# Kernel tuning notes

Measured on AMD Instinct MI355X. Metric: run time of the kernel, lower is better.

Reference implementation:

```python
import jax, jax.numpy as jnp
import numpy as np
import math

D = 2048
NH = 16       # query heads
NKV = 4       # kv heads (GQA)
HD = 128
SOFTCLAMP = 50.0
ROPE_BASE = 10000.0
B = 4
SQ_VLM = 1024
SQ_ACT = 64
S_CACHE = 256


def _heads(x, n):
    # [B,S,n*HD] -> [B,n,S,HD]
    b, s, _ = x.shape
    return x.reshape(b, s, n, HD).transpose(0, 2, 1, 3)


def _rope_cos_sin(pos):
    # pos: [B,S] int -> cos,sin [B,1,S,HD]
    inv_freq = 1.0 / (ROPE_BASE ** (jnp.arange(0, HD, 2, dtype=jnp.float32) / HD))
    freqs = pos.astype(jnp.float32)[..., None] * inv_freq  # [B,S,HD/2]
    emb = jnp.concatenate([freqs, freqs], axis=-1)         # [B,S,HD]
    return jnp.cos(emb)[:, None], jnp.sin(emb)[:, None]


def _apply_rope(x, cos, sin):
    # x: [B,H,S,HD]
    x1, x2 = x[..., : HD // 2], x[..., HD // 2 :]
    rot = jnp.concatenate([-x2, x1], axis=-1)
    return x * cos + rot * sin


def setup_inputs() -> dict:
    key = jax.random.key(0)
    ks = jax.random.split(key, 16)
    sc = lambda d: 1.0 / math.sqrt(d)
    inp = {
        'attention_mask': jnp.zeros((B, 1, SQ_VLM + SQ_ACT, S_CACHE + SQ_VLM + SQ_ACT), jnp.float32),
        'pos_vlm': jnp.broadcast_to(jnp.arange(S_CACHE, S_CACHE + SQ_VLM, dtype=jnp.int32), (B, SQ_VLM)),
        'pos_action': jnp.broadcast_to(jnp.arange(S_CACHE + SQ_VLM, S_CACHE + SQ_VLM + SQ_ACT, dtype=jnp.int32), (B, SQ_ACT)),
        'h_vlm': jax.random.normal(ks[0], (B, SQ_VLM, D), jnp.float32),
        'h_action': jax.random.normal(ks[1], (B, SQ_ACT, D), jnp.float32),
        'k_cache': jax.random.normal(ks[2], (B, NKV, S_CACHE, HD), jnp.float32),
        'v_cache': jax.random.normal(ks[3], (B, NKV, S_CACHE, HD), jnp.float32),
        'Wq_vlm': jax.random.normal(ks[4], (D, NH * HD), jnp.float32) * sc(D),
        'Wk_vlm': jax.random.normal(ks[5], (D, NKV * HD), jnp.float32) * sc(D),
        'Wv_vlm': jax.random.normal(ks[6], (D, NKV * HD), jnp.float32) * sc(D),
        'Wq_act': jax.random.normal(ks[7], (D, NH * HD), jnp.float32) * sc(D),
        'Wk_act': jax.random.normal(ks[8], (D, NKV * HD), jnp.float32) * sc(D),
        'Wv_act': jax.random.normal(ks[9], (D, NKV * HD), jnp.float32) * sc(D),
        'Wo_act': jax.random.normal(ks[10], (NH * HD, D), jnp.float32) * sc(NH * HD),
    }
    return inp


def reference(attention_mask, pos_vlm, pos_action, h_vlm, h_action, k_cache, v_cache,
              Wq_vlm, Wk_vlm, Wv_vlm, Wq_act, Wk_act, Wv_act, Wo_act):
    group = NH // NKV

    def qkv(h, pos, Wq, Wk, Wv):
        q = _heads(h @ Wq, NH)
        k = _heads(h @ Wk, NKV)
        v = _heads(h @ Wv, NKV)
        cos, sin = _rope_cos_sin(pos)
        return _apply_rope(q, cos, sin), _apply_rope(k, cos, sin), v

    q_v, k_v, v_v = qkv(h_vlm, pos_vlm, Wq_vlm, Wk_vlm, Wv_vlm)
    q_a, k_a, v_a = qkv(h_action, pos_action, Wq_act, Wk_act, Wv_act)

    # repeat_kv (GQA) on every KV source, cached mixture first (append_non_active order)
    rep = lambda t: jnp.repeat(t, group, axis=1)  # [B,NKV,S,HD] -> [B,NH,S,HD]
    k = jnp.concatenate([rep(k_cache), rep(k_v), rep(k_a)], axis=2)
    v = jnp.concatenate([rep(v_cache), rep(v_v), rep(v_a)], axis=2)
    q = jnp.concatenate([q_v, q_a], axis=2)  # [B,NH,Sq,HD]

    scores = jnp.einsum('bhqd,bhkd->bhqk', q, k) / math.sqrt(HD)
    scores = jnp.tanh(scores / SOFTCLAMP) * SOFTCLAMP + attention_mask
    w = jax.nn.softmax(scores.astype(jnp.float32), axis=-1).astype(q.dtype)
    out = jnp.einsum('bhqk,bhkd->bhqd', w, v)
    out = out.transpose(0, 2, 1, 3).reshape(B, SQ_VLM + SQ_ACT, NH * HD)

    # split by q_lens; 'vlm' is in post_attn_skip_names -> no o_proj, dropped
    out_action = out[:, SQ_VLM:, :]
    return out_action @ Wo_act
```

## Files before the change

kernel.cpp:

```cpp
#include <hip/hip_runtime.h>
#include <cmath>

#define NH 16
#define NKV 4
#define HD 128
#define DMODEL 2048
#define BB 4
#define SQV 1024
#define SQA 64
#define SCACHE 256
#define STOT 1344
#define SQTOT 1088
#define NSPLIT 21

typedef unsigned short u16;
typedef __attribute__((ext_vector_type(8))) short short8;
typedef __attribute__((ext_vector_type(4))) float f32x4;

__device__ __forceinline__ float b2f(u16 u) {
    union { float f; unsigned int i; } x; x.i = ((unsigned int)u) << 16; return x.f;
}
__device__ __forceinline__ u16 f2b(float f) {
    unsigned int x = __float_as_uint(f);
    x = x + 0x7fffu + ((x >> 16) & 1u);
    return (u16)(x >> 16);
}

__device__ __forceinline__ void gload16(const void* g, void* l) {
    __builtin_amdgcn_global_load_lds((const __attribute__((address_space(1))) void*)g,
                                     (__attribute__((address_space(3))) void*)l, 16, 0, 0);
}

__device__ __forceinline__ void transpose_body(const float* in, u16* out, int N,
                                               int bx, int by) {
    __shared__ __align__(16) u16 t[64 * 66];
    int n0 = bx * 64, k0 = by * 64;
    int tid = threadIdx.x;
    int r = tid >> 3;
    int c8 = (tid & 7) * 8;
#pragma unroll
    for (int h = 0; h < 2; h++) {
        int k = r + h * 32;
        const float* f = in + (size_t)(k0 + k) * N + n0 + c8;
        float4 a = *(const float4*)f, b = *(const float4*)(f + 4);
        u16 vv[8] = {f2b(a.x), f2b(a.y), f2b(a.z), f2b(a.w),
                     f2b(b.x), f2b(b.y), f2b(b.z), f2b(b.w)};
#pragma unroll
        for (int j = 0; j < 8; j++) t[(c8 + j) * 66 + k] = vv[j];
    }
    __syncthreads();
#pragma unroll
    for (int h = 0; h < 2; h++) {
        int n = r + h * 32;
        short8 v;
#pragma unroll
        for (int j = 0; j < 8; j++) ((u16*)&v)[j] = t[n * 66 + c8 + j];
        *(short8*)(out + (size_t)(n0 + n) * 2048 + k0 + c8) = v;
    }
}

__device__ __forceinline__ void transpose_vc(const float* vc, u16* VT, int idx) {
    __shared__ __align__(16) u16 tv[64 * 66];
    int bkv = idx >> 3, t8 = idx & 7;
    int key0 = (t8 >> 1) * 64, d0 = (t8 & 1) * 64;
    const float* in = vc + ((size_t)bkv * SCACHE + key0) * HD + d0;
    u16* out = VT + ((size_t)bkv * HD + d0) * STOT + key0;
    int tid = threadIdx.x;
    int r = tid >> 3, c8 = (tid & 7) * 8;
#pragma unroll
    for (int h = 0; h < 2; h++) {
        int k = r + h * 32;
        const float* f = in + (size_t)k * HD + c8;
        float4 a = *(const float4*)f, b = *(const float4*)(f + 4);
        u16 vv[8] = {f2b(a.x), f2b(a.y), f2b(a.z), f2b(a.w),
                     f2b(b.x), f2b(b.y), f2b(b.z), f2b(b.w)};
#pragma unroll
        for (int j = 0; j < 8; j++) tv[(c8 + j) * 66 + k] = vv[j];
    }
    __syncthreads();
#pragma unroll
    for (int h = 0; h < 2; h++) {
        int d = r + h * 32;
        short8 v;
#pragma unroll
        for (int j = 0; j < 8; j++) ((u16*)&v)[j] = tv[d * 66 + c8 + j];
        *(short8*)(out + (size_t)d * STOT + c8) = v;
    }
}

__global__ void k_prep(const float* __restrict__ mask,
                       const float* __restrict__ kc, const float* __restrict__ vc,
                       const float* __restrict__ hv, const float* __restrict__ ha,
                       const float* __restrict__ w0, u16* __restrict__ o0,
                       const float* __restrict__ w1, u16* __restrict__ o1,
                       const float* __restrict__ w2, u16* __restrict__ o2,
                       const float* __restrict__ w3, u16* __restrict__ o3,
                       const float* __restrict__ w4, u16* __restrict__ o4,
                       const float* __restrict__ w5, u16* __restrict__ o5,
                       float* __restrict__ cosT, float* __restrict__ sinT,
                       u16* __restrict__ maskS, u16* __restrict__ K_all, u16* __restrict__ VT_all,
                       u16* __restrict__ hv16, u16* __restrict__ ha16) {
    int gx = blockIdx.x, tid = threadIdx.x;
    if (gx < 3072) {
        if (gx < 256)        transpose_body(w0, o0, 512,  gx & 7,  gx >> 3);
        else if (gx < 512)   { int g = gx - 256;  transpose_body(w1, o1, 512,  g & 7,  g >> 3); }
        else if (gx < 768)   { int g = gx - 512;  transpose_body(w2, o2, 512,  g & 7,  g >> 3); }
        else if (gx < 1024)  { int g = gx - 768;  transpose_body(w3, o3, 512,  g & 7,  g >> 3); }
        else if (gx < 2048)  { int g = gx - 1024; transpose_body(w4, o4, 2048, g & 31, g >> 5); }
        else                 { int g = gx - 2048; transpose_body(w5, o5, 2048, g & 31, g >> 5); }
        return;
    }
    int bx = gx - 3072;
    if (bx < 336) {
        int i = bx * 256 + tid;
        if (i < STOT * 64) {
            int p = i >> 6, j = i & 63;
            float inv = __expf(-(float)j * (9.210340371976184f / 64.0f));
            float ang = (float)p * inv;
            cosT[i] = cosf(ang);
            sinT[i] = sinf(ang);
        }
    } else if (bx < 1680) {
        int i = (bx - 336) * 256 + tid;
        int b = i / (SQA * STOT);
        int r = i % (SQA * STOT);
        size_t s = (size_t)b * SQTOT * STOT + (size_t)SQV * STOT + r;
        maskS[i] = f2b(mask[s]);
    } else if (bx < 1936) {
        int i = (bx - 1680) * 256 + tid;
        int e = i * 8;
        int bk = e / (SCACHE * HD);
        int off = e % (SCACHE * HD);
        size_t dst = (size_t)bk * STOT * HD + off;
        const float* fk = kc + e;
        u16 tk[8];
#pragma unroll
        for (int j = 0; j < 8; j++) tk[j] = f2b(fk[j]);
        *(short8*)(K_all + dst) = *(short8*)tk;
    } else if (bx < 6032) {
        int i = (bx - 1936) * 256 + tid;
        int e = i * 8;
        const float* f = hv + e;
        float4 a = *(const float4*)f, b = *(const float4*)(f + 4);
        u16 t[8] = {f2b(a.x), f2b(a.y), f2b(a.z), f2b(a.w),
                    f2b(b.x), f2b(b.y), f2b(b.z), f2b(b.w)};
        *(short8*)(hv16 + e) = *(short8*)t;
    } else if (bx < 6288) {
        int i = (bx - 6032) * 256 + tid;
        int e = i * 8;
        const float* f = ha + e;
        float4 a = *(const float4*)f, b = *(const float4*)(f + 4);
        u16 t[8] = {f2b(a.x), f2b(a.y), f2b(a.z), f2b(a.w),
                    f2b(b.x), f2b(b.y), f2b(b.z), f2b(b.w)};
        *(short8*)(ha16 + e) = *(short8*)t;
    } else {
        transpose_vc(vc, VT_all, bx - 6288);
    }
}

__global__ __launch_bounds__(256) void k_gemm_qkv(
    const u16* __restrict__ Avlm, const u16* __restrict__ Aact,
    const u16* __restrict__ WkvT, const u16* __restrict__ WvvT,
    const u16* __restrict__ WqaT, const u16* __restrict__ WkaT, const u16* __restrict__ WvaT,
    const int* __restrict__ pos_vlm, const int* __restrict__ pos_act,
    const float* __restrict__ cosT, const float* __restrict__ sinT,
    u16* __restrict__ Qbuf, u16* __restrict__ K_all, u16* __restrict__ VT_all) {
    __shared__ __align__(16) u16 smem[2 * 12288];
    int tid = threadIdx.x;
    int w = tid >> 6, lane = tid & 63;
    int la = lane & 15, lg = lane >> 4;
    int wm = (w & 1) * 32;
    int c2 = w >> 1;
    int ntab[4] = {c2 * 2, c2 * 2 + 1, c2 * 2 + 4, c2 * 2 + 5};

    const u16* A; const u16* Bt; int m0, n0;
    int path;
    int head;
    int bid = blockIdx.x;
    if (bid < 512) {
        m0 = (bid & 63) * 64;
        int yy = bid >> 6;
        path = (yy < 4) ? 0 : 1;
        head = yy & 3;
        n0 = head * 128;
        A = Avlm;
        Bt = (path == 0) ? WkvT : WvvT;
    } else {
        int g = bid - 512;
        m0 = (g & 3) * 64;
        int ny = g >> 2;
        A = Aact;
        if (ny < 16)      { path = 2; head = ny;      Bt = WqaT; n0 = ny * 128; }
        else if (ny < 20) { path = 3; head = ny - 16; Bt = WkaT; n0 = (ny - 16) * 128; }
        else              { path = 4; head = ny - 20; Bt = WvaT; n0 = (ny - 20) * 128; }
    }

    f32x4 acc[2][4];
#pragma unroll
    for (int i = 0; i < 2; i++)
#pragma unroll
        for (int j = 0; j < 4; j++) acc[i][j] = (f32x4){0.f, 0.f, 0.f, 0.f};

    int srow = tid >> 3;
    int scsrc = (((tid & 7) * 16) ^ ((srow & 7) << 4)) >> 1;

#define STAGE_QKV(CB, KB) do {                                                        \
        u16* Ab_ = smem + (CB) * 12288;                                               \
        u16* Bb_ = Ab_ + 4096;                                                        \
        _Pragma("unroll")                                                             \
        for (int h = 0; h < 2; h++)                                                   \
            gload16(A + (size_t)(m0 + srow + h * 32) * DMODEL + (KB) + scsrc,         \
                    Ab_ + h * 2048 + tid * 8);                                        \
        _Pragma("unroll")                                                             \
        for (int h = 0; h < 4; h++)                                                   \
            gload16(Bt + (size_t)(n0 + srow + h * 32) * DMODEL + (KB) + scsrc,        \
                    Bb_ + h * 2048 + tid * 8);                                        \
    } while (0)

    STAGE_QKV(0, 0);
    int cur = 0;
    int swr = (la & 7) << 3;
    for (int kb = 0; kb < DMODEL; kb += 64) {
        if (kb + 64 < DMODEL) {
            STAGE_QKV(cur ^ 1, kb + 64);
            asm volatile("s_waitcnt vmcnt(6)" ::: "memory");
        } else {
            asm volatile("s_waitcnt vmcnt(0)" ::: "memory");
        }
        __builtin_amdgcn_s_barrier();
        asm volatile("" ::: "memory");
        const u16* Ac = smem + cur * 12288;
        const u16* Bc = Ac + 4096;
#pragma unroll
        for (int kk = 0; kk < 2; kk++) {
            short8 af[2], bf[4];
            int cc = (kk * 32 + lg * 8) ^ swr;
#pragma unroll
            for (int mt = 0; mt < 2; mt++)
                af[mt] = *(const short8*)&Ac[(wm + mt * 16 + la) * 64 + cc];
#pragma unroll
            for (int nt = 0; nt < 4; nt++)
                bf[nt] = *(const short8*)&Bc[(ntab[nt] * 16 + la) * 64 + cc];
#pragma unroll
            for (int mt = 0; mt < 2; mt++)
#pragma unroll
                for (int nt = 0; nt < 4; nt++)
                    acc[mt][nt] = __builtin_amdgcn_mfma_f32_16x16x32_bf16(af[mt], bf[nt], acc[mt][nt], 0, 0, 0);
        }
        __builtin_amdgcn_s_barrier();
        cur ^= 1;
    }
#undef STAGE_QKV

#pragma unroll
    for (int mt = 0; mt < 2; mt++) {
#pragma unroll
        for (int r = 0; r < 4; r++) {
            int gm = m0 + wm + mt * 16 + lg * 4 + r;
            if (path <= 1) {
                int b = gm >> 10, s = gm & 1023;
                if (path == 0) {
                    size_t base = ((size_t)(b * NKV + head) * STOT + SCACHE + s) * HD;
                    int pos = pos_vlm[gm];
#pragma unroll
                    for (int i = 0; i < 2; i++) {
                        int dlo = ntab[i] * 16 + la;
                        float x1 = acc[mt][i][r], x2 = acc[mt][i + 2][r];
                        float cs = cosT[pos * 64 + dlo], sn = sinT[pos * 64 + dlo];
                        K_all[base + dlo]      = f2b(x1 * cs - x2 * sn);
                        K_all[base + dlo + 64] = f2b(x2 * cs + x1 * sn);
                    }
                } else {
                    size_t vt = ((size_t)(b * NKV + head) * HD) * STOT + SCACHE + s;
#pragma unroll
                    for (int i = 0; i < 4; i++) {
                        int d = ntab[i] * 16 + la;
                        VT_all[vt + (size_t)d * STOT] = f2b(acc[mt][i][r]);
                    }
                }
            } else {
                int b = gm >> 6, s = gm & 63;
                if (path == 2) {
                    int pos = pos_act[gm];
                    size_t qb = ((size_t)(b * NH + head) * SQA + s) * HD;
#pragma unroll
                    for (int i = 0; i < 2; i++) {
                        int dlo = ntab[i] * 16 + la;
                        float x1 = acc[mt][i][r], x2 = acc[mt][i + 2][r];
                        float cs = cosT[pos * 64 + dlo], sn = sinT[pos * 64 + dlo];
                        Qbuf[qb + dlo]      = f2b(x1 * cs - x2 * sn);
                        Qbuf[qb + dlo + 64] = f2b(x2 * cs + x1 * sn);
                    }
                } else if (path == 3) {
                    int pos = pos_act[gm];
                    size_t base = ((size_t)(b * NKV + head) * STOT + SCACHE + SQV + s) * HD;
#pragma unroll
                    for (int i = 0; i < 2; i++) {
                        int dlo = ntab[i] * 16 + la;
                        float x1 = acc[mt][i][r], x2 = acc[mt][i + 2][r];
                        float cs = cosT[pos * 64 + dlo], sn = sinT[pos * 64 + dlo];
                        K_all[base + dlo]      = f2b(x1 * cs - x2 * sn);
                        K_all[base + dlo + 64] = f2b(x2 * cs + x1 * sn);
                    }
                } else {
                    size_t vt = ((size_t)(b * NKV + head) * HD) * STOT + SCACHE + SQV + s;
#pragma unroll
                    for (int i = 0; i < 4; i++) {
                        int d = ntab[i] * 16 + la;
                        VT_all[vt + (size_t)d * STOT] = f2b(acc[mt][i][r]);
                    }
                }
            }
        }
    }
}

__global__ __launch_bounds__(256) void k_attn_split(
    const u16* __restrict__ Qbuf, const u16* __restrict__ K_all, const u16* __restrict__ VT_all,
    const u16* __restrict__ maskS, u16* __restrict__ po, float* __restrict__ pml) {
    int h = blockIdx.x, b = blockIdx.y, p = blockIdx.z;
    int bh = b * NH + h;
    int kvh = h >> 2;
    const u16* Kb  = K_all  + (size_t)(b * NKV + kvh) * STOT * HD;
    const u16* VTb = VT_all + (size_t)(b * NKV + kvh) * HD * STOT;
    const u16* Qb  = Qbuf + (size_t)bh * SQA * HD;
    int tid = threadIdx.x, w = tid >> 6, lane = tid & 63;
    int la = lane & 15, lg = lane >> 4;
    __shared__ __align__(16) u16 Ks[64 * 128];
    __shared__ __align__(16) u16 Vt[128 * 64];
    __shared__ __align__(16) u16 Ps[4][16 * 72];

    int kr = tid >> 4;
    int ksw = (((tid & 15) * 16) ^ ((kr & 7) << 4)) >> 1;
    int vr = tid >> 3;
    int vsw = (((tid & 7) * 16) ^ ((vr & 7) << 4)) >> 1;
#pragma unroll
    for (int hh = 0; hh < 4; hh++)
        gload16(Kb + (size_t)(p * 64 + kr + hh * 16) * HD + ksw, &Ks[hh * 2048 + tid * 8]);
#pragma unroll
    for (int hh = 0; hh < 4; hh++)
        gload16(VTb + (size_t)(vr + hh * 32) * STOT + p * 64 + vsw, &Vt[hh * 2048 + tid * 8]);

    short8 qf[4];
#pragma unroll
    for (int kk = 0; kk < 4; kk++)
        qf[kk] = *(const short8*)(Qb + (size_t)(w * 16 + la) * HD + kk * 32 + lg * 8);
    u16 mreg[4][4];
#pragma unroll
    for (int nt = 0; nt < 4; nt++)
#pragma unroll
        for (int r = 0; r < 4; r++)
            mreg[nt][r] = maskS[((size_t)(b * SQA + w * 16 + lg * 4 + r)) * STOT +
                                p * 64 + nt * 16 + la];

    asm volatile("s_waitcnt vmcnt(0)" ::: "memory");
    __builtin_amdgcn_s_barrier();
    asm volatile("" ::: "memory");

    int swr = (la & 7) << 3;
    const float scl = 0.08838834764831845f;
    f32x4 s_acc[4];
#pragma unroll
    for (int nt = 0; nt < 4; nt++) s_acc[nt] = (f32x4){0.f, 0.f, 0.f, 0.f};
    __builtin_amdgcn_s_setprio(1);
#pragma unroll
    for (int kk = 0; kk < 4; kk++) {
        int cc = (kk * 32 + lg * 8) ^ swr;
#pragma unroll
        for (int nt = 0; nt < 4; nt++) {
            short8 kf = *(const short8*)&Ks[(nt * 16 + la) * 128 + cc];
            s_acc[nt] = __builtin_amdgcn_mfma_f32_16x16x32_bf16(qf[kk], kf, s_acc[nt], 0, 0, 0);
        }
    }
    __builtin_amdgcn_s_setprio(0);
    float sc[4][4];
#pragma unroll
    for (int nt = 0; nt < 4; nt++) {
#pragma unroll
        for (int r = 0; r < 4; r++) {
            float sv = s_acc[nt][r] * scl;
            float x = sv * 0.02f;
            float t = __expf(-2.0f * fabsf(x));
            float th = __fdividef(1.0f - t, 1.0f + t);
            sv = copysignf(th, x) * 50.0f;
            sv += b2f(mreg[nt][r]);
            sc[nt][r] = sv;
        }
    }
    float m_fin[4], l_fin[4];
#pragma unroll
    for (int r = 0; r < 4; r++) {
        float mx = fmaxf(fmaxf(sc[0][r], sc[1][r]), fmaxf(sc[2][r], sc[3][r]));
#pragma unroll
        for (int sh = 1; sh < 16; sh <<= 1) mx = fmaxf(mx, __shfl_xor(mx, sh, 64));
        float rowsum = 0.f;
#pragma unroll
        for (int nt = 0; nt < 4; nt++) {
            float pv = __expf(sc[nt][r] - mx);
            Ps[w][(lg * 4 + r) * 72 + nt * 16 + la] = f2b(pv);
            rowsum += pv;
        }
#pragma unroll
        for (int sh = 1; sh < 16; sh <<= 1) rowsum += __shfl_xor(rowsum, sh, 64);
        m_fin[r] = mx;
        l_fin[r] = rowsum;
    }
    f32x4 o_acc[8];
#pragma unroll
    for (int nt = 0; nt < 8; nt++) o_acc[nt] = (f32x4){0.f, 0.f, 0.f, 0.f};
    __builtin_amdgcn_s_setprio(1);
#pragma unroll
    for (int kk = 0; kk < 2; kk++) {
        short8 pf = *(const short8*)&Ps[w][la * 72 + kk * 32 + lg * 8];
        int cc = (kk * 32 + lg * 8) ^ swr;
#pragma unroll
        for (int nt = 0; nt < 8; nt++) {
            short8 vf = *(const short8*)&Vt[(nt * 16 + la) * 64 + cc];
            o_acc[nt] = __builtin_amdgcn_mfma_f32_16x16x32_bf16(pf, vf, o_acc[nt], 0, 0, 0);
        }
    }
    __builtin_amdgcn_s_setprio(0);
#pragma unroll
    for (int nt = 0; nt < 8; nt++) {
#pragma unroll
        for (int r = 0; r < 4; r++) {
            int sq = w * 16 + lg * 4 + r;
            po[(((size_t)p * 64 + bh) * 64 + sq) * 128 + nt * 16 + la] = f2b(o_acc[nt][r]);
        }
    }
    if (la == 0) {
#pragma unroll
        for (int r = 0; r < 4; r++) {
            int sq = w * 16 + lg * 4 + r;
            size_t mlb = (((size_t)p * 64 + bh) * 64 + sq) * 2;
            pml[mlb] = m_fin[r];
            pml[mlb + 1] = l_fin[r];
        }
    }
}

__global__ __launch_bounds__(256) void k_attn_red(
    const u16* __restrict__ po, const float* __restrict__ pml, u16* __restrict__ AO) {
    int h = blockIdx.x, b = blockIdx.y, qz = blockIdx.z * 16;
    int bh = b * NH + h;
    __shared__ float wgt[NSPLIT][16];
    int tid = threadIdx.x;
    if (tid < 16) {
        int q = qz + tid;
        float m[NSPLIT], l[NSPLIT], M = -3e38f;
#pragma unroll
        for (int p = 0; p < NSPLIT; p++) {
            size_t mlb = (((size_t)p * 64 + bh) * 64 + q) * 2;
            m[p] = pml[mlb]; l[p] = pml[mlb + 1];
            M = fmaxf(M, m[p]);
        }
        float L = 0.f;
#pragma unroll
        for (int p = 0; p < NSPLIT; p++) L += l[p] * __expf(m[p] - M);
        float inv = 1.0f / L;
#pragma unroll
        for (int p = 0; p < NSPLIT; p++) wgt[p][tid] = __expf(m[p] - M) * inv;
    }
    __syncthreads();
    for (int e = tid; e < 16 * 128; e += 256) {
        int q = qz + (e >> 7), d = e & 127;
        float s = 0.f;
#pragma unroll
        for (int p = 0; p < NSPLIT; p++)
            s += b2f(po[(((size_t)p * 64 + bh) * 64 + q) * 128 + d]) * wgt[p][e >> 7];
        AO[((size_t)(b * SQA + q)) * 2048 + h * HD + d] = f2b(s);
    }
}

__global__ __launch_bounds__(256) void k_gemm_out(
    const u16* __restrict__ A, const u16* __restrict__ WoT, float* __restrict__ out) {
    __shared__ __align__(16) u16 smem[2 * 6144];
    int m0 = blockIdx.x * 32, n0 = blockIdx.y * 64;
    int tid = threadIdx.x;
    int w = tid >> 6, lane = tid & 63;
    int la = lane & 15, lg = lane >> 4;
    int wm = (w & 1) * 16, wn = (w >> 1) * 32;
    f32x4 acc[2];
#pragma unroll
    for (int j = 0; j < 2; j++) acc[j] = (f32x4){0.f, 0.f, 0.f, 0.f};

    int srow = tid >> 3;
    int scsrc = (((tid & 7) * 16) ^ ((srow & 7) << 4)) >> 1;

#define STAGE_OUT(CB, KB) do {                                                        \
        u16* Ab_ = smem + (CB) * 6144;                                                \
        u16* Bb_ = Ab_ + 2048;                                                        \
        gload16(A + (size_t)(m0 + srow) * DMODEL + (KB) + scsrc, Ab_ + tid * 8);      \
        _Pragma("unroll")                                                             \
        for (int h = 0; h < 2; h++)                                                   \
            gload16(WoT + (size_t)(n0 + srow + h * 32) * DMODEL + (KB) + scsrc,       \
                    Bb_ + h * 2048 + tid * 8);                                        \
    } while (0)

    STAGE_OUT(0, 0);
    int cur = 0;
    int swr = (la & 7) << 3;
    for (int kb = 0; kb < DMODEL; kb += 64) {
        if (kb + 64 < DMODEL) {
            STAGE_OUT(cur ^ 1, kb + 64);
            asm volatile("s_waitcnt vmcnt(3)" ::: "memory");
        } else {
            asm volatile("s_waitcnt vmcnt(0)" ::: "memory");
        }
        __builtin_amdgcn_s_barrier();
        asm volatile("" ::: "memory");
        const u16* Ac = smem + cur * 6144;
        const u16* Bc = Ac + 2048;
#pragma unroll
        for (int kk = 0; kk < 2; kk++) {
            int cc = (kk * 32 + lg * 8) ^ swr;
            short8 af = *(const short8*)&Ac[(wm + la) * 64 + cc];
            short8 bf[2];
#pragma unroll
            for (int nt = 0; nt < 2; nt++) bf[nt] = *(const short8*)&Bc[(wn + nt * 16 + la) * 64 + cc];
#pragma unroll
            for (int nt = 0; nt < 2; nt++)
                acc[nt] = __builtin_amdgcn_mfma_f32_16x16x32_bf16(af, bf[nt], acc[nt], 0, 0, 0);
        }
        __builtin_amdgcn_s_barrier();
        cur ^= 1;
    }
#undef STAGE_OUT

#pragma unroll
    for (int r = 0; r < 4; r++) {
        int gm = m0 + wm + lg * 4 + r;
#pragma unroll
        for (int nt = 0; nt < 2; nt++)
            out[(size_t)gm * DMODEL + n0 + wn + nt * 16 + la] = acc[nt][r];
    }
}

extern "C" void kernel_launch(void* const* d_in, const int* in_sizes, int n_in,
                              void* d_out, int out_size, void* d_ws, size_t ws_size,
                              hipStream_t stream) {
    (void)in_sizes; (void)n_in; (void)out_size;
    const float* mask    = (const float*)d_in[0];
    const int*   pos_vlm = (const int*)d_in[1];
    const int*   pos_act = (const int*)d_in[2];
    const float* h_vlm   = (const float*)d_in[3];
    const float* h_act   = (const float*)d_in[4];
    const float* k_cache = (const float*)d_in[5];
    const float* v_cache = (const float*)d_in[6];
    const float* Wk_vlm  = (const float*)d_in[8];
    const float* Wv_vlm  = (const float*)d_in[9];
    const float* Wq_act  = (const float*)d_in[10];
    const float* Wk_act  = (const float*)d_in[11];
    const float* Wv_act  = (const float*)d_in[12];
    const float* Wo_act  = (const float*)d_in[13];

    const size_t NEED = 80183296;
    if (ws_size < NEED) return;
    char* ws = (char*)d_ws;
    float* cosT  = (float*)(ws + 0);
    float* sinT  = (float*)(ws + 344064);
    u16* K_all   = (u16*)(ws + 688128);
    u16* VT_all  = (u16*)(ws + 6193152);
    u16* Qbuf    = (u16*)(ws + 11698176);
    u16* AO      = (u16*)(ws + 12746752);
    u16* WkvT    = (u16*)(ws + 13795328);
    u16* WvvT    = (u16*)(ws + 15892480);
    u16* WqaT    = (u16*)(ws + 17989632);
    u16* WkaT    = (u16*)(ws + 26378240);
    u16* WvaT    = (u16*)(ws + 28475392);
    u16* WoT     = (u16*)(ws + 30572544);
    u16* po      = (u16*)(ws + 38961152);
    float* pml   = (float*)(ws + 60981248);
    u16* maskS   = (u16*)(ws + 61669376);
    u16* hv16    = (u16*)(ws + 62357504);
    u16* ha16    = (u16*)(ws + 79134720);

    hipLaunchKernelGGL(k_prep, dim3(9488), dim3(256), 0, stream,
                       mask, k_cache, v_cache, h_vlm, h_act,
                       Wk_vlm, WkvT, Wv_vlm, WvvT, Wk_act, WkaT, Wv_act, WvaT,
                       Wq_act, WqaT, Wo_act, WoT,
                       cosT, sinT, maskS, K_all, VT_all, hv16, ha16);
    hipLaunchKernelGGL(k_gemm_qkv, dim3(608), dim3(256), 0, stream,
                       hv16, ha16, WkvT, WvvT, WqaT, WkaT, WvaT,
                       pos_vlm, pos_act, cosT, sinT, Qbuf, K_all, VT_all);
    hipLaunchKernelGGL(k_attn_split, dim3(16, 4, NSPLIT), dim3(256), 0, stream,
                       Qbuf, K_all, VT_all, maskS, po, pml);
    hipLaunchKernelGGL(k_attn_red, dim3(16, 4, 4), dim3(256), 0, stream, po, pml, AO);
    hipLaunchKernelGGL(k_gemm_out, dim3(8, 32), dim3(256), 0, stream, AO, WoT, (float*)d_out);
}
```

Measured before the change: 232.7 us.

## Triple-buffer QKV GEMM and loop attention splits over three KV chunks

The QKV GEMM switches from double to triple buffering, issuing loads two stages ahead and dropping the trailing barrier per iteration. The split attention kernel now processes three 64-key chunks per block with online softmax (lazy rescale when the max grows by more than 8) and double-buffered K/V staging, cutting splits from 21 to 7. This reduces partial-output traffic and the reduction work, but gives fewer attention blocks and more LDS per GEMM block, which may lower occupancy.

```diff
diff --git a/kernel.cpp b/kernel.cpp
--- a/kernel.cpp
+++ b/kernel.cpp
@@ -11,7 +11,7 @@
 #define SCACHE 256
 #define STOT 1344
 #define SQTOT 1088
-#define NSPLIT 21
+#define NSPLIT 7
 
 typedef unsigned short u16;
 typedef __attribute__((ext_vector_type(8))) short short8;
@@ -165,7 +165,7 @@
     const int* __restrict__ pos_vlm, const int* __restrict__ pos_act,
     const float* __restrict__ cosT, const float* __restrict__ sinT,
     u16* __restrict__ Qbuf, u16* __restrict__ K_all, u16* __restrict__ VT_all) {
-    __shared__ __align__(16) u16 smem[2 * 12288];
+    __shared__ __align__(16) u16 smem[3 * 12288];
     int tid = threadIdx.x;
     int w = tid >> 6, lane = tid & 63;
     int la = lane & 15, lg = lane >> 4;
@@ -204,8 +204,8 @@
     int srow = tid >> 3;
     int scsrc = (((tid & 7) * 16) ^ ((srow & 7) << 4)) >> 1;
 
-#define STAGE_QKV(CB, KB) do {                                                        \
-        u16* Ab_ = smem + (CB) * 12288;                                               \
+#define STAGE_QKV(BASE, KB) do {                                                      \
+        u16* Ab_ = (BASE);                                                            \
         u16* Bb_ = Ab_ + 4096;                                                        \
         _Pragma("unroll")                                                             \
         for (int h = 0; h < 2; h++)                                                   \
@@ -217,19 +217,17 @@
                     Bb_ + h * 2048 + tid * 8);                                        \
     } while (0)
 
-    STAGE_QKV(0, 0);
-    int cur = 0;
+    STAGE_QKV(smem, 0);
+    STAGE_QKV(smem + 12288, 64);
+    int bufR = 0, bufS = 2;
     int swr = (la & 7) << 3;
-    for (int kb = 0; kb < DMODEL; kb += 64) {
-        if (kb + 64 < DMODEL) {
-            STAGE_QKV(cur ^ 1, kb + 64);
-            asm volatile("s_waitcnt vmcnt(6)" ::: "memory");
-        } else {
-            asm volatile("s_waitcnt vmcnt(0)" ::: "memory");
-        }
+    for (int t = 0; t < 32; ++t) {
+        if (t < 31) asm volatile("s_waitcnt vmcnt(6)" ::: "memory");
+        else        asm volatile("s_waitcnt vmcnt(0)" ::: "memory");
         __builtin_amdgcn_s_barrier();
         asm volatile("" ::: "memory");
-        const u16* Ac = smem + cur * 12288;
+        if (t < 30) STAGE_QKV(smem + bufS * 12288, (t + 2) * 64);
+        const u16* Ac = smem + bufR * 12288;
         const u16* Bc = Ac + 4096;
 #pragma unroll
         for (int kk = 0; kk < 2; kk++) {
@@ -247,8 +245,8 @@
                 for (int nt = 0; nt < 4; nt++)
                     acc[mt][nt] = __builtin_amdgcn_mfma_f32_16x16x32_bf16(af[mt], bf[nt], acc[mt][nt], 0, 0, 0);
         }
-        __builtin_amdgcn_s_barrier();
-        cur ^= 1;
+        bufR = (bufR == 2) ? 0 : bufR + 1;
+        bufS = (bufS == 2) ? 0 : bufS + 1;
     }
 #undef STAGE_QKV
 
@@ -326,100 +324,125 @@
     const u16* Qb  = Qbuf + (size_t)bh * SQA * HD;
     int tid = threadIdx.x, w = tid >> 6, lane = tid & 63;
     int la = lane & 15, lg = lane >> 4;
-    __shared__ __align__(16) u16 Ks[64 * 128];
-    __shared__ __align__(16) u16 Vt[128 * 64];
+    __shared__ __align__(16) u16 Ks[2][64 * 128];
+    __shared__ __align__(16) u16 Vt[2][128 * 64];
     __shared__ __align__(16) u16 Ps[4][16 * 72];
 
     int kr = tid >> 4;
     int ksw = (((tid & 15) * 16) ^ ((kr & 7) << 4)) >> 1;
     int vr = tid >> 3;
     int vsw = (((tid & 7) * 16) ^ ((vr & 7) << 4)) >> 1;
-#pragma unroll
-    for (int hh = 0; hh < 4; hh++)
-        gload16(Kb + (size_t)(p * 64 + kr + hh * 16) * HD + ksw, &Ks[hh * 2048 + tid * 8]);
-#pragma unroll
-    for (int hh = 0; hh < 4; hh++)
-        gload16(VTb + (size_t)(vr + hh * 32) * STOT + p * 64 + vsw, &Vt[hh * 2048 + tid * 8]);
-
+
+#define ASTAGE(CB, G) do {                                                            \
+        _Pragma("unroll")                                                             \
+        for (int hh = 0; hh < 4; hh++)                                                \
+            gload16(Kb + (size_t)((G) * 64 + kr + hh * 16) * HD + ksw,                \
+                    &Ks[CB][hh * 2048 + tid * 8]);                                    \
+        _Pragma("unroll")                                                             \
+        for (int hh = 0; hh < 4; hh++)                                                \
+            gload16(VTb + (size_t)(vr + hh * 32) * STOT + (G) * 64 + vsw,             \
+                    &Vt[CB][hh * 2048 + tid * 8]);                                    \
+    } while (0)
+
+    ASTAGE(0, p * 3);
     short8 qf[4];
 #pragma unroll
     for (int kk = 0; kk < 4; kk++)
         qf[kk] = *(const short8*)(Qb + (size_t)(w * 16 + la) * HD + kk * 32 + lg * 8);
-    u16 mreg[4][4];
-#pragma unroll
-    for (int nt = 0; nt < 4; nt++)
-#pragma unroll
-        for (int r = 0; r < 4; r++)
-            mreg[nt][r] = maskS[((size_t)(b * SQA + w * 16 + lg * 4 + r)) * STOT +
-                                p * 64 + nt * 16 + la];
-
-    asm volatile("s_waitcnt vmcnt(0)" ::: "memory");
-    __builtin_amdgcn_s_barrier();
-    asm volatile("" ::: "memory");
-
+    f32x4 o_acc[8];
+#pragma unroll
+    for (int nt = 0; nt < 8; nt++) o_acc[nt] = (f32x4){0.f, 0.f, 0.f, 0.f};
+    float m_run[4], l_run[4];
+#pragma unroll
+    for (int r = 0; r < 4; r++) { m_run[r] = -3e38f; l_run[r] = 0.f; }
+
+    int cur = 0;
     int swr = (la & 7) << 3;
     const float scl = 0.08838834764831845f;
-    f32x4 s_acc[4];
-#pragma unroll
-    for (int nt = 0; nt < 4; nt++) s_acc[nt] = (f32x4){0.f, 0.f, 0.f, 0.f};
-    __builtin_amdgcn_s_setprio(1);
-#pragma unroll
-    for (int kk = 0; kk < 4; kk++) {
-        int cc = (kk * 32 + lg * 8) ^ swr;
+    for (int c = 0; c < 3; c++) {
+        int g = p * 3 + c;
+        u16 mreg[4][4];
+#pragma unroll
+        for (int nt = 0; nt < 4; nt++)
+#pragma unroll
+            for (int r = 0; r < 4; r++)
+                mreg[nt][r] = maskS[((size_t)(b * SQA + w * 16 + lg * 4 + r)) * STOT +
+                                    g * 64 + nt * 16 + la];
+        if (c < 2) {
+            ASTAGE(cur ^ 1, g + 1);
+            asm volatile("s_waitcnt vmcnt(8)" ::: "memory");
+        } else {
+            asm volatile("s_waitcnt vmcnt(0)" ::: "memory");
+        }
+        __builtin_amdgcn_s_barrier();
+        asm volatile("" ::: "memory");
+        f32x4 s_acc[4];
+#pragma unroll
+        for (int nt = 0; nt < 4; nt++) s_acc[nt] = (f32x4){0.f, 0.f, 0.f, 0.f};
+        __builtin_amdgcn_s_setprio(1);
+#pragma unroll
+        for (int kk = 0; kk < 4; kk++) {
+            int cc = (kk * 32 + lg * 8) ^ swr;
+#pragma unroll
+            for (int nt = 0; nt < 4; nt++) {
+                short8 kf = *(const short8*)&Ks[cur][(nt * 16 + la) * 128 + cc];
+                s_acc[nt] = __builtin_amdgcn_mfma_f32_16x16x32_bf16(qf[kk], kf, s_acc[nt], 0, 0, 0);
+            }
+        }
+        __builtin_amdgcn_s_setprio(0);
+        float sc[4][4];
 #pragma unroll
         for (int nt = 0; nt < 4; nt++) {
-            short8 kf = *(const short8*)&Ks[(nt * 16 + la) * 128 + cc];
-            s_acc[nt] = __builtin_amdgcn_mfma_f32_16x16x32_bf16(qf[kk], kf, s_acc[nt], 0, 0, 0);
-        }
-    }
-    __builtin_amdgcn_s_setprio(0);
-    float sc[4][4];
-#pragma unroll
-    for (int nt = 0; nt < 4; nt++) {
+#pragma unroll
+            for (int r = 0; r < 4; r++) {
+                float sv = s_acc[nt][r] * scl;
+                float x = sv * 0.02f;
+                float t = __expf(-2.0f * fabsf(x));
+                float th = __fdividef(1.0f - t, 1.0f + t);
+                sv = copysignf(th, x) * 50.0f;
+                sv += b2f(mreg[nt][r]);
+                sc[nt][r] = sv;
+            }
+        }
 #pragma unroll
         for (int r = 0; r < 4; r++) {
-            float sv = s_acc[nt][r] * scl;
-            float x = sv * 0.02f;
-            float t = __expf(-2.0f * fabsf(x));
-            float th = __fdividef(1.0f - t, 1.0f + t);
-            sv = copysignf(th, x) * 50.0f;
-            sv += b2f(mreg[nt][r]);
-            sc[nt][r] = sv;
-        }
-    }
-    float m_fin[4], l_fin[4];
-#pragma unroll
-    for (int r = 0; r < 4; r++) {
-        float mx = fmaxf(fmaxf(sc[0][r], sc[1][r]), fmaxf(sc[2][r], sc[3][r]));
-#pragma unroll
-        for (int sh = 1; sh < 16; sh <<= 1) mx = fmaxf(mx, __shfl_xor(mx, sh, 64));
-        float rowsum = 0.f;
-#pragma unroll
-        for (int nt = 0; nt < 4; nt++) {
-            float pv = __expf(sc[nt][r] - mx);
-            Ps[w][(lg * 4 + r) * 72 + nt * 16 + la] = f2b(pv);
-            rowsum += pv;
-        }
-#pragma unroll
-        for (int sh = 1; sh < 16; sh <<= 1) rowsum += __shfl_xor(rowsum, sh, 64);
-        m_fin[r] = mx;
-        l_fin[r] = rowsum;
-    }
-    f32x4 o_acc[8];
-#pragma unroll
-    for (int nt = 0; nt < 8; nt++) o_acc[nt] = (f32x4){0.f, 0.f, 0.f, 0.f};
-    __builtin_amdgcn_s_setprio(1);
-#pragma unroll
-    for (int kk = 0; kk < 2; kk++) {
-        short8 pf = *(const short8*)&Ps[w][la * 72 + kk * 32 + lg * 8];
-        int cc = (kk * 32 + lg * 8) ^ swr;
-#pragma unroll
-        for (int nt = 0; nt < 8; nt++) {
-            short8 vf = *(const short8*)&Vt[(nt * 16 + la) * 64 + cc];
-            o_acc[nt] = __builtin_amdgcn_mfma_f32_16x16x32_bf16(pf, vf, o_acc[nt], 0, 0, 0);
-        }
-    }
-    __builtin_amdgcn_s_setprio(0);
+            float mx = fmaxf(fmaxf(sc[0][r], sc[1][r]), fmaxf(sc[2][r], sc[3][r]));
+#pragma unroll
+            for (int sh = 1; sh < 16; sh <<= 1) mx = fmaxf(mx, __shfl_xor(mx, sh, 64));
+            if (mx > m_run[r] + 8.0f) {
+                float alpha = __expf(m_run[r] - mx);
+                m_run[r] = mx;
+                l_run[r] *= alpha;
+#pragma unroll
+                for (int nt = 0; nt < 8; nt++) o_acc[nt][r] *= alpha;
+            }
+            float rowsum = 0.f;
+#pragma unroll
+            for (int nt = 0; nt < 4; nt++) {
+                float pv = __expf(sc[nt][r] - m_run[r]);
+                Ps[w][(lg * 4 + r) * 72 + nt * 16 + la] = f2b(pv);
+                rowsum += pv;
+            }
+#pragma unroll
+            for (int sh = 1; sh < 16; sh <<= 1) rowsum += __shfl_xor(rowsum, sh, 64);
+            l_run[r] += rowsum;
+        }
+        __builtin_amdgcn_s_setprio(1);
+#pragma unroll
+        for (int kk = 0; kk < 2; kk++) {
+            short8 pf = *(const short8*)&Ps[w][la * 72 + kk * 32 + lg * 8];
+            int cc = (kk * 32 + lg * 8) ^ swr;
+#pragma unroll
+            for (int nt = 0; nt < 8; nt++) {
+                short8 vf = *(const short8*)&Vt[cur][(nt * 16 + la) * 64 + cc];
+                o_acc[nt] = __builtin_amdgcn_mfma_f32_16x16x32_bf16(pf, vf, o_acc[nt], 0, 0, 0);
+            }
+        }
+        __builtin_amdgcn_s_setprio(0);
+        __builtin_amdgcn_s_barrier();
+        cur ^= 1;
+    }
+#undef ASTAGE
 #pragma unroll
     for (int nt = 0; nt < 8; nt++) {
 #pragma unroll
@@ -433,8 +456,8 @@
         for (int r = 0; r < 4; r++) {
             int sq = w * 16 + lg * 4 + r;
             size_t mlb = (((size_t)p * 64 + bh) * 64 + sq) * 2;
-            pml[mlb] = m_fin[r];
-            pml[mlb + 1] = l_fin[r];
+            pml[mlb] = m_run[r];
+            pml[mlb + 1] = l_run[r];
         }
     }
 }
@@ -554,7 +577,7 @@
     const float* Wv_act  = (const float*)d_in[12];
     const float* Wo_act  = (const float*)d_in[13];
 
-    const size_t NEED = 80183296;
+    const size_t NEED = 65273856;
     if (ws_size < NEED) return;
     char* ws = (char*)d_ws;
     float* cosT  = (float*)(ws + 0);
@@ -570,10 +593,10 @@
     u16* WvaT    = (u16*)(ws + 28475392);
     u16* WoT     = (u16*)(ws + 30572544);
     u16* po      = (u16*)(ws + 38961152);
-    float* pml   = (float*)(ws + 60981248);
-    u16* maskS   = (u16*)(ws + 61669376);
-    u16* hv16    = (u16*)(ws + 62357504);
-    u16* ha16    = (u16*)(ws + 79134720);
+    float* pml   = (float*)(ws + 46301184);
+    u16* maskS   = (u16*)(ws + 46759936);
+    u16* hv16    = (u16*)(ws + 47448064);
+    u16* ha16    = (u16*)(ws + 64225280);
 
     hipLaunchKernelGGL(k_prep, dim3(9488), dim3(256), 0, stream,
                        mask, k_cache, v_cache, h_vlm, h_act,
```

Result: no change. 234.4 us (+0.7%).
